# Kernel optimization log

Measured on AMD Instinct MI355X. Metric: run time of the kernel, lower is better.

Reference implementation:

```python
import jax, jax.numpy as jnp
import numpy as np

V, E, H, L, P, N = 500000, 128, 128, 10, 10, 50
SCALE = 1e-4


def setup_inputs() -> dict:
    key = jax.random.key(0)
    ks = jax.random.split(key, 10)
    initrange = 0.5 / E
    return {
        "phr_inds": jax.random.randint(ks[0], (L,), 0, V),
        "pos_inds": jax.random.randint(ks[1], (P, L), 0, V),
        "neg_inds": jax.random.randint(ks[2], (N, L), 0, V),
        "u_emb": jax.random.uniform(ks[3], (V, E), minval=-initrange, maxval=initrange, dtype=jnp.float32),
        "v_emb": jax.random.uniform(ks[4], (V, E), minval=-initrange, maxval=initrange, dtype=jnp.float32),
        "w_ih": jax.random.uniform(ks[5], (3 * H, E), minval=-SCALE, maxval=SCALE, dtype=jnp.float32),
        "w_hh": jax.random.uniform(ks[6], (3 * H, H), minval=-SCALE, maxval=SCALE, dtype=jnp.float32),
        "b_ih": jax.random.uniform(ks[7], (3 * H,), minval=-SCALE, maxval=SCALE, dtype=jnp.float32),
        "b_hh": jax.random.uniform(ks[8], (3 * H,), minval=-SCALE, maxval=SCALE, dtype=jnp.float32),
        "h0": jax.random.uniform(ks[9], (H,), minval=-SCALE, maxval=SCALE, dtype=jnp.float32),
    }


def _gru_last_hidden(x, h0, w_ih, w_hh, b_ih, b_hh):
    # x: [B, L, E] -> last hidden state [B, H]; torch GRU gate order (r, z, n)
    B = x.shape[0]
    gi = jnp.einsum('ble,ge->blg', x, w_ih) + b_ih  # input projections precomputed [B, L, 3H]
    h = jnp.broadcast_to(h0, (B, h0.shape[-1]))

    def step(h, gi_t):
        gh = h @ w_hh.T + b_hh
        ir, iz, in_ = jnp.split(gi_t, 3, axis=-1)
        hr, hz, hn = jnp.split(gh, 3, axis=-1)
        r = jax.nn.sigmoid(ir + hr)
        z = jax.nn.sigmoid(iz + hz)
        n = jnp.tanh(in_ + r * hn)
        return (1.0 - z) * n + z * h, None

    h, _ = jax.lax.scan(step, h, jnp.swapaxes(gi, 0, 1))  # scan over time
    return h


def reference(phr_inds, pos_inds, neg_inds, u_emb, v_emb, w_ih, w_hh, b_ih, b_hh, h0):
    rnn_size = h0.shape[-1]
    phr_x = u_emb[phr_inds][None]   # [1, L, E] (center phrase uses u table)
    pos_x = v_emb[pos_inds]         # [P, L, E]
    neg_x = v_emb[neg_inds]         # [N, L, E]
    x = jnp.concatenate([phr_x, pos_x, neg_x], axis=0)  # batch all GRU calls together
    enc = _gru_last_hidden(x, h0, w_ih, w_hh, b_ih, b_hh)
    node = enc[0]
    n_pos = pos_inds.shape[0]
    pos_e, neg_e = enc[1:1 + n_pos], enc[1 + n_pos:]
    # dot_product_sum(exp=False): sum_i <node, pos_i> / rnn_size
    pos_loss = ((node * pos_e).sum(-1) / rnn_size).sum()
    # dot_product_sum(exp=True): exp(s) masked to s>0, then summed
    s = (node * neg_e).sum(-1) / rnn_size
    neg_sum = (jnp.exp(s) * (s > 0.0).astype(s.dtype)).sum()
    neg_loss = -jnp.log(1.0 + neg_sum)
    return -(neg_loss + pos_loss)
```

## Files before the change

### kernel.cpp

```cpp
#include <hip/hip_runtime.h>
#include <hip/hip_bf16.h>
#include <math.h>

#define V_SZ 500000
#define E_SZ 128
#define H_SZ 128
#define L_SZ 10
#define P_SZ 10
#define N_SZ 50
#define NSEQ (P_SZ + N_SZ)
#define NBLK 60
#define TPB  384

#define FLAG_STRIDE 16
#define SLOT_STRIDE 16
#define FLAG_MAGIC  0x9E370000u

#define GI_STR 388
#define XS_STR 136
#define SLAB_ROWS 192

typedef __attribute__((ext_vector_type(8))) short bf16x8;
typedef __attribute__((ext_vector_type(4))) float f32x4;

#define MFMA(a, b, c) __builtin_amdgcn_mfma_f32_16x16x32_bf16((a), (b), (c), 0, 0, 0)

__device__ __forceinline__ float sigmoidf(float x) {
    return 1.0f / (1.0f + expf(-x));
}

__device__ __forceinline__ unsigned short f2bf(float f) {
    unsigned u = __float_as_uint(f);
    u += 0x7FFFu + ((u >> 16) & 1u);
    return (unsigned short)(u >> 16);
}

__global__ __launch_bounds__(TPB) void gru_fused(
    const int*   __restrict__ phr_inds,
    const int*   __restrict__ pos_inds,
    const int*   __restrict__ neg_inds,
    const float* __restrict__ u_emb,
    const float* __restrict__ v_emb,
    const float* __restrict__ w_ih,
    const float* __restrict__ w_hh,
    const float* __restrict__ b_ih,
    const float* __restrict__ b_hh,
    const float* __restrict__ h0,
    float*       __restrict__ slots,
    unsigned*    __restrict__ flags,
    float*       __restrict__ out)
{
    __shared__ __align__(16) unsigned short stage[SLAB_ROWS * E_SZ];
    __shared__ __align__(16) unsigned short xs_bf16[2][16 * XS_STR];
    __shared__ __align__(16) float          gi_all[2][16 * GI_STR];
    __shared__ __align__(16) float          gh_s[2][3 * H_SZ];
    __shared__ __align__(16) unsigned short hs_bf16[2][H_SZ];
    __shared__ __align__(16) float          node[2][H_SZ];

    const int bj   = blockIdx.x;
    const int seqB = bj + 1;
    const int t    = threadIdx.x;
    const int lane = t & 63;
    const int wv   = t >> 6;
    const int kg   = lane >> 4;
    const int col  = lane & 15;
    const int arow = wv * 64 + col;

    for (int i = t; i < 2 * L_SZ * 32; i += TPB) {
        const int r  = i >> 5;
        const int e4 = i & 31;
        const int g  = (r < L_SZ) ? 0 : 1;
        const int l  = (r < L_SZ) ? r : r - L_SZ;
        int idx; const float* emb;
        if (g == 0)             { idx = phr_inds[l];                       emb = u_emb; }
        else if (seqB <= P_SZ)  { idx = pos_inds[(seqB - 1) * L_SZ + l];   emb = v_emb; }
        else                    { idx = neg_inds[(seqB - 1 - P_SZ) * L_SZ + l]; emb = v_emb; }
        const float4 v = *reinterpret_cast<const float4*>(emb + (size_t)idx * E_SZ + e4 * 4);
        short4 s4;
        s4.x = (short)f2bf(v.x); s4.y = (short)f2bf(v.y);
        s4.z = (short)f2bf(v.z); s4.w = (short)f2bf(v.w);
        *reinterpret_cast<short4*>((char*)&xs_bf16[g][0] + l * (XS_STR * 2) + e4 * 8) = s4;
    }

    const int gseq = t >> 7;
    const int gu   = t & 127;
    float bih_r = 0.f, bih_z = 0.f, bih_n = 0.f;
    float bhh_r = 0.f, bhh_z = 0.f, bhh_n = 0.f;
    float h_reg = 0.f;
    if (t < 2 * H_SZ) {
        bih_r = b_ih[gu]; bih_z = b_ih[gu + 128]; bih_n = b_ih[gu + 256];
        bhh_r = b_hh[gu]; bhh_z = b_hh[gu + 128]; bhh_n = b_hh[gu + 256];
        h_reg = h0[gu];
        hs_bf16[gseq][gu] = f2bf(h_reg);
    }

    bf16x8 aih[4][4], ahh[4][4];
    #pragma unroll
    for (int m = 0; m < 2; ++m) {
        const float* W = (m == 0) ? w_ih : w_hh;
        #pragma unroll
        for (int s = 0; s < 2; ++s) {
            #pragma unroll 8
            for (int q = 0; q < (SLAB_ROWS * E_SZ / 4) / TPB; ++q) {
                const int fi = q * TPB + t;
                const int lr = fi >> 5;
                const int e4 = fi & 31;
                const float4 v = *reinterpret_cast<const float4*>(
                    W + (size_t)(s * SLAB_ROWS + lr) * E_SZ + e4 * 4);
                short4 s4;
                s4.x = (short)f2bf(v.x); s4.y = (short)f2bf(v.y);
                s4.z = (short)f2bf(v.z); s4.w = (short)f2bf(v.w);
                const int byte = (lr * 256 + e4 * 8) ^ ((lr & 7) << 4);
                *reinterpret_cast<short4*>((char*)stage + byte) = s4;
            }
            __syncthreads();

            if (wv >= s * 3 && wv < (s + 1) * 3) {
                const int lr0 = arow - s * SLAB_ROWS;
                #pragma unroll
                for (int mb = 0; mb < 4; ++mb) {
                    #pragma unroll
                    for (int kb = 0; kb < 4; ++kb) {
                        const int lr   = lr0 + mb * 16;
                        const int byte = (lr * 256 + kb * 64 + kg * 16) ^ ((lr & 7) << 4);
                        const bf16x8 f = *reinterpret_cast<const bf16x8*>((const char*)stage + byte);
                        if (m == 0) aih[mb][kb] = f;
                        else        ahh[mb][kb] = f;
                    }
                }
            }
            __syncthreads();
        }
    }

    #pragma unroll
    for (int g = 0; g < 2; ++g) {
        f32x4 g0 = {0.f,0.f,0.f,0.f}, g1 = {0.f,0.f,0.f,0.f};
        f32x4 g2 = {0.f,0.f,0.f,0.f}, g3 = {0.f,0.f,0.f,0.f};
        #pragma unroll
        for (int kb = 0; kb < 4; ++kb) {
            const bf16x8 xb = *reinterpret_cast<const bf16x8*>(
                (const char*)&xs_bf16[g][0] + col * (XS_STR * 2) + kb * 64 + kg * 16);
            g0 = MFMA(aih[0][kb], xb, g0);
            g1 = MFMA(aih[1][kb], xb, g1);
            g2 = MFMA(aih[2][kb], xb, g2);
            g3 = MFMA(aih[3][kb], xb, g3);
        }
        const int rb = wv * 64 + kg * 4;
        *reinterpret_cast<f32x4*>(&gi_all[g][col * GI_STR + rb     ]) = g0;
        *reinterpret_cast<f32x4*>(&gi_all[g][col * GI_STR + rb + 16]) = g1;
        *reinterpret_cast<f32x4*>(&gi_all[g][col * GI_STR + rb + 32]) = g2;
        *reinterpret_cast<f32x4*>(&gi_all[g][col * GI_STR + rb + 48]) = g3;
    }

    for (int l = 0; l < L_SZ; ++l) {
        f32x4 a0 = {0.f,0.f,0.f,0.f}, a1 = {0.f,0.f,0.f,0.f};
        f32x4 a2 = {0.f,0.f,0.f,0.f}, a3 = {0.f,0.f,0.f,0.f};
        #pragma unroll
        for (int kb = 0; kb < 4; ++kb) {
            const bf16x8 bh = *reinterpret_cast<const bf16x8*>(
                (const char*)&hs_bf16[col & 1][0] + kb * 64 + kg * 16);
            a0 = MFMA(ahh[0][kb], bh, a0);
            a1 = MFMA(ahh[1][kb], bh, a1);
            a2 = MFMA(ahh[2][kb], bh, a2);
            a3 = MFMA(ahh[3][kb], bh, a3);
        }
        if (col < 2) {
            const int rb = wv * 64 + kg * 4;
            *reinterpret_cast<f32x4*>(&gh_s[col][rb     ]) = a0;
            *reinterpret_cast<f32x4*>(&gh_s[col][rb + 16]) = a1;
            *reinterpret_cast<f32x4*>(&gh_s[col][rb + 32]) = a2;
            *reinterpret_cast<f32x4*>(&gh_s[col][rb + 48]) = a3;
        }
        __syncthreads();

        if (t < 2 * H_SZ) {
            const float* gi = &gi_all[gseq][l * GI_STR];
            const float* gh = &gh_s[gseq][0];
            const float r = sigmoidf(gi[gu      ] + bih_r + (gh[gu      ] + bhh_r));
            const float z = sigmoidf(gi[gu + 128] + bih_z + (gh[gu + 128] + bhh_z));
            const float n = tanhf  (gi[gu + 256] + bih_n + r * (gh[gu + 256] + bhh_n));
            h_reg = (1.0f - z) * n + z * h_reg;
            if (l < L_SZ - 1) hs_bf16[gseq][gu] = f2bf(h_reg);
            else              node[gseq][gu]   = h_reg;
        }
        __syncthreads();
    }

    if (t >= 64) return;

    float d = node[0][t] * node[1][t] + node[0][t + 64] * node[1][t + 64];
    #pragma unroll
    for (int off = 32; off > 0; off >>= 1) d += __shfl_down(d, off);
    const float s_own = d * (1.0f / (float)H_SZ);

    if (bj != 0) {
        if (t == 0) {
            slots[bj * SLOT_STRIDE] = s_own;
            __threadfence();
            atomicExch(&flags[bj * FLAG_STRIDE], FLAG_MAGIC + (unsigned)bj);
        }
        return;
    }

    float sv = 0.0f;
    if (t == 0) sv = s_own;
    else if (t < NSEQ) {
        const unsigned want = FLAG_MAGIC + (unsigned)t;
        while (atomicAdd(&flags[t * FLAG_STRIDE], 0u) != want) {
            __builtin_amdgcn_s_sleep(2);
        }
        __threadfence();
        sv = slots[t * SLOT_STRIDE];
    }

    float vp = 0.0f, vn = 0.0f;
    if (t < P_SZ)      vp = sv;
    else if (t < NSEQ) vn = (sv > 0.0f) ? expf(sv) : 0.0f;

    #pragma unroll
    for (int off = 32; off > 0; off >>= 1) {
        vp += __shfl_down(vp, off);
        vn += __shfl_down(vn, off);
    }
    if (t == 0) {
        out[0] = logf(1.0f + vn) - vp;
    }
}

extern "C" void kernel_launch(void* const* d_in, const int* in_sizes, int n_in,
                              void* d_out, int out_size, void* d_ws, size_t ws_size,
                              hipStream_t stream) {
    const int*   phr_inds = (const int*)  d_in[0];
    const int*   pos_inds = (const int*)  d_in[1];
    const int*   neg_inds = (const int*)  d_in[2];
    const float* u_emb    = (const float*)d_in[3];
    const float* v_emb    = (const float*)d_in[4];
    const float* w_ih     = (const float*)d_in[5];
    const float* w_hh     = (const float*)d_in[6];
    const float* b_ih     = (const float*)d_in[7];
    const float* b_hh     = (const float*)d_in[8];
    const float* h0       = (const float*)d_in[9];

    float*    slots = (float*)d_ws;
    unsigned* flags = (unsigned*)((char*)d_ws + 16384);

    gru_fused<<<NBLK, TPB, 0, stream>>>(phr_inds, pos_inds, neg_inds,
                                        u_emb, v_emb, w_ih, w_hh, b_ih, b_hh, h0,
                                        slots, flags, (float*)d_out);
}
```

Measured before the change: 23.02 us.

## Repartition GRU gates per wave so gate math stays in registers, one barrier per step

Switches to 8 waves, each owning 16 hidden units across all three gates (r,z,n). The gate nonlinearities are then computed directly from MFMA accumulators in the lanes that hold them, instead of round-tripping gh through shared memory with a second barrier. The hidden state is double-buffered so each timestep needs a single __syncthreads. Weight staging is done in one full 384-row pass per matrix, gi is stored with biases folded in, and the gi buffer reuses the staging LDS. This risks more threads per block and heavier per-lane elementwise work, since only 2 of 16 columns do the gate math.

After: 32.53 us. 41.3% more time.

```diff
diff --git a/kernel.cpp b/kernel.cpp
--- a/kernel.cpp
+++ b/kernel.cpp
@@ -10,15 +10,14 @@
 #define N_SZ 50
 #define NSEQ (P_SZ + N_SZ)
 #define NBLK 60
-#define TPB  384
+#define TPB  512
 
 #define FLAG_STRIDE 16
 #define SLOT_STRIDE 16
 #define FLAG_MAGIC  0x9E370000u
 
-#define GI_STR 388
-#define XS_STR 136
-#define SLAB_ROWS 192
+#define XS_STR  136
+#define GI_USTR 132
 
 typedef __attribute__((ext_vector_type(8))) short bf16x8;
 typedef __attribute__((ext_vector_type(4))) float f32x4;
@@ -50,12 +49,12 @@
     unsigned*    __restrict__ flags,
     float*       __restrict__ out)
 {
-    __shared__ __align__(16) unsigned short stage[SLAB_ROWS * E_SZ];
+    __shared__ __align__(16) unsigned short stage_u[384 * E_SZ];
     __shared__ __align__(16) unsigned short xs_bf16[2][16 * XS_STR];
-    __shared__ __align__(16) float          gi_all[2][16 * GI_STR];
-    __shared__ __align__(16) float          gh_s[2][3 * H_SZ];
-    __shared__ __align__(16) unsigned short hs_bf16[2][H_SZ];
+    __shared__ __align__(16) unsigned short hs_bf16[2][2][H_SZ];
     __shared__ __align__(16) float          node[2][H_SZ];
+
+    float* gi_all = (float*)stage_u;
 
     const int bj   = blockIdx.x;
     const int seqB = bj + 1;
@@ -64,7 +63,8 @@
     const int wv   = t >> 6;
     const int kg   = lane >> 4;
     const int col  = lane & 15;
-    const int arow = wv * 64 + col;
+    const int ur   = wv * 16;
+    const int ub   = ur + kg * 4;
 
     for (int i = t; i < 2 * L_SZ * 32; i += TPB) {
         const int r  = i >> 5;
@@ -82,109 +82,107 @@
         *reinterpret_cast<short4*>((char*)&xs_bf16[g][0] + l * (XS_STR * 2) + e4 * 8) = s4;
     }
 
-    const int gseq = t >> 7;
-    const int gu   = t & 127;
-    float bih_r = 0.f, bih_z = 0.f, bih_n = 0.f;
-    float bhh_r = 0.f, bhh_z = 0.f, bhh_n = 0.f;
-    float h_reg = 0.f;
-    if (t < 2 * H_SZ) {
-        bih_r = b_ih[gu]; bih_z = b_ih[gu + 128]; bih_n = b_ih[gu + 256];
-        bhh_r = b_hh[gu]; bhh_z = b_hh[gu + 128]; bhh_n = b_hh[gu + 256];
-        h_reg = h0[gu];
-        hs_bf16[gseq][gu] = f2bf(h_reg);
-    }
-
-    bf16x8 aih[4][4], ahh[4][4];
+    const f32x4 bihr = *reinterpret_cast<const f32x4*>(b_ih + ub);
+    const f32x4 bihz = *reinterpret_cast<const f32x4*>(b_ih + 128 + ub);
+    const f32x4 bihn = *reinterpret_cast<const f32x4*>(b_ih + 256 + ub);
+    const f32x4 bhhr = *reinterpret_cast<const f32x4*>(b_hh + ub);
+    const f32x4 bhhz = *reinterpret_cast<const f32x4*>(b_hh + 128 + ub);
+    const f32x4 bhhn = *reinterpret_cast<const f32x4*>(b_hh + 256 + ub);
+    f32x4 hreg = *reinterpret_cast<const f32x4*>(h0 + ub);
+
+    if (col < 2) {
+        short4 s4;
+        s4.x = (short)f2bf(hreg[0]); s4.y = (short)f2bf(hreg[1]);
+        s4.z = (short)f2bf(hreg[2]); s4.w = (short)f2bf(hreg[3]);
+        *reinterpret_cast<short4*>(&hs_bf16[0][col][ub]) = s4;
+    }
+
+    bf16x8 aih[3][4], ahh[3][4];
     #pragma unroll
     for (int m = 0; m < 2; ++m) {
         const float* W = (m == 0) ? w_ih : w_hh;
+        #pragma unroll 8
+        for (int q = 0; q < (384 * E_SZ / 4) / TPB; ++q) {
+            const int fi = q * TPB + t;
+            const int lr = fi >> 5;
+            const int e4 = fi & 31;
+            const float4 v = *reinterpret_cast<const float4*>(W + (size_t)lr * E_SZ + e4 * 4);
+            short4 s4;
+            s4.x = (short)f2bf(v.x); s4.y = (short)f2bf(v.y);
+            s4.z = (short)f2bf(v.z); s4.w = (short)f2bf(v.w);
+            const int byte = (lr * 256 + e4 * 8) ^ ((lr & 7) << 4);
+            *reinterpret_cast<short4*>((char*)stage_u + byte) = s4;
+        }
+        __syncthreads();
+
         #pragma unroll
-        for (int s = 0; s < 2; ++s) {
-            #pragma unroll 8
-            for (int q = 0; q < (SLAB_ROWS * E_SZ / 4) / TPB; ++q) {
-                const int fi = q * TPB + t;
-                const int lr = fi >> 5;
-                const int e4 = fi & 31;
-                const float4 v = *reinterpret_cast<const float4*>(
-                    W + (size_t)(s * SLAB_ROWS + lr) * E_SZ + e4 * 4);
-                short4 s4;
-                s4.x = (short)f2bf(v.x); s4.y = (short)f2bf(v.y);
-                s4.z = (short)f2bf(v.z); s4.w = (short)f2bf(v.w);
-                const int byte = (lr * 256 + e4 * 8) ^ ((lr & 7) << 4);
-                *reinterpret_cast<short4*>((char*)stage + byte) = s4;
+        for (int gate = 0; gate < 3; ++gate) {
+            const int lr = gate * H_SZ + ur + col;
+            #pragma unroll
+            for (int kb = 0; kb < 4; ++kb) {
+                const int byte = (lr * 256 + kb * 64 + kg * 16) ^ ((lr & 7) << 4);
+                const bf16x8 f = *reinterpret_cast<const bf16x8*>((const char*)stage_u + byte);
+                if (m == 0) aih[gate][kb] = f;
+                else        ahh[gate][kb] = f;
             }
-            __syncthreads();
-
-            if (wv >= s * 3 && wv < (s + 1) * 3) {
-                const int lr0 = arow - s * SLAB_ROWS;
-                #pragma unroll
-                for (int mb = 0; mb < 4; ++mb) {
-                    #pragma unroll
-                    for (int kb = 0; kb < 4; ++kb) {
-                        const int lr   = lr0 + mb * 16;
-                        const int byte = (lr * 256 + kb * 64 + kg * 16) ^ ((lr & 7) << 4);
-                        const bf16x8 f = *reinterpret_cast<const bf16x8*>((const char*)stage + byte);
-                        if (m == 0) aih[mb][kb] = f;
-                        else        ahh[mb][kb] = f;
-                    }
-                }
-            }
-            __syncthreads();
-        }
+        }
+        __syncthreads();
     }
 
     #pragma unroll
     for (int g = 0; g < 2; ++g) {
-        f32x4 g0 = {0.f,0.f,0.f,0.f}, g1 = {0.f,0.f,0.f,0.f};
-        f32x4 g2 = {0.f,0.f,0.f,0.f}, g3 = {0.f,0.f,0.f,0.f};
+        f32x4 ar = {0.f,0.f,0.f,0.f}, az = {0.f,0.f,0.f,0.f}, an = {0.f,0.f,0.f,0.f};
         #pragma unroll
         for (int kb = 0; kb < 4; ++kb) {
             const bf16x8 xb = *reinterpret_cast<const bf16x8*>(
                 (const char*)&xs_bf16[g][0] + col * (XS_STR * 2) + kb * 64 + kg * 16);
-            g0 = MFMA(aih[0][kb], xb, g0);
-            g1 = MFMA(aih[1][kb], xb, g1);
-            g2 = MFMA(aih[2][kb], xb, g2);
-            g3 = MFMA(aih[3][kb], xb, g3);
-        }
-        const int rb = wv * 64 + kg * 4;
-        *reinterpret_cast<f32x4*>(&gi_all[g][col * GI_STR + rb     ]) = g0;
-        *reinterpret_cast<f32x4*>(&gi_all[g][col * GI_STR + rb + 16]) = g1;
-        *reinterpret_cast<f32x4*>(&gi_all[g][col * GI_STR + rb + 32]) = g2;
-        *reinterpret_cast<f32x4*>(&gi_all[g][col * GI_STR + rb + 48]) = g3;
-    }
-
+            ar = MFMA(aih[0][kb], xb, ar);
+            az = MFMA(aih[1][kb], xb, az);
+            an = MFMA(aih[2][kb], xb, an);
+        }
+        if (col < L_SZ) {
+            const int base = (g * L_SZ + col) * 3;
+            *reinterpret_cast<f32x4*>(&gi_all[(base + 0) * GI_USTR + ub]) = ar + bihr;
+            *reinterpret_cast<f32x4*>(&gi_all[(base + 1) * GI_USTR + ub]) = az + bihz;
+            *reinterpret_cast<f32x4*>(&gi_all[(base + 2) * GI_USTR + ub]) = an + bihn;
+        }
+    }
+    __syncthreads();
+
+    int p = 0;
     for (int l = 0; l < L_SZ; ++l) {
-        f32x4 a0 = {0.f,0.f,0.f,0.f}, a1 = {0.f,0.f,0.f,0.f};
-        f32x4 a2 = {0.f,0.f,0.f,0.f}, a3 = {0.f,0.f,0.f,0.f};
+        f32x4 ar = {0.f,0.f,0.f,0.f}, az = {0.f,0.f,0.f,0.f}, an = {0.f,0.f,0.f,0.f};
         #pragma unroll
         for (int kb = 0; kb < 4; ++kb) {
             const bf16x8 bh = *reinterpret_cast<const bf16x8*>(
-                (const char*)&hs_bf16[col & 1][0] + kb * 64 + kg * 16);
-            a0 = MFMA(ahh[0][kb], bh, a0);
-            a1 = MFMA(ahh[1][kb], bh, a1);
-            a2 = MFMA(ahh[2][kb], bh, a2);
-            a3 = MFMA(ahh[3][kb], bh, a3);
+                (const char*)&hs_bf16[p][col & 1][0] + kb * 64 + kg * 16);
+            ar = MFMA(ahh[0][kb], bh, ar);
+            az = MFMA(ahh[1][kb], bh, az);
+            an = MFMA(ahh[2][kb], bh, an);
         }
         if (col < 2) {
-            const int rb = wv * 64 + kg * 4;
-            *reinterpret_cast<f32x4*>(&gh_s[col][rb     ]) = a0;
-            *reinterpret_cast<f32x4*>(&gh_s[col][rb + 16]) = a1;
-            *reinterpret_cast<f32x4*>(&gh_s[col][rb + 32]) = a2;
-            *reinterpret_cast<f32x4*>(&gh_s[col][rb + 48]) = a3;
+            const int base = (col * L_SZ + l) * 3;
+            const f32x4 gr = *reinterpret_cast<const f32x4*>(&gi_all[(base + 0) * GI_USTR + ub]);
+            const f32x4 gz = *reinterpret_cast<const f32x4*>(&gi_all[(base + 1) * GI_USTR + ub]);
+            const f32x4 gn = *reinterpret_cast<const f32x4*>(&gi_all[(base + 2) * GI_USTR + ub]);
+            #pragma unroll
+            for (int j = 0; j < 4; ++j) {
+                const float r = sigmoidf(gr[j] + (ar[j] + bhhr[j]));
+                const float z = sigmoidf(gz[j] + (az[j] + bhhz[j]));
+                const float n = tanhf  (gn[j] + r * (an[j] + bhhn[j]));
+                hreg[j] = (1.0f - z) * n + z * hreg[j];
+            }
+            if (l < L_SZ - 1) {
+                short4 s4;
+                s4.x = (short)f2bf(hreg[0]); s4.y = (short)f2bf(hreg[1]);
+                s4.z = (short)f2bf(hreg[2]); s4.w = (short)f2bf(hreg[3]);
+                *reinterpret_cast<short4*>(&hs_bf16[p ^ 1][col][ub]) = s4;
+            } else {
+                *reinterpret_cast<f32x4*>(&node[col][ub]) = hreg;
+            }
         }
         __syncthreads();
-
-        if (t < 2 * H_SZ) {
-            const float* gi = &gi_all[gseq][l * GI_STR];
-            const float* gh = &gh_s[gseq][0];
-            const float r = sigmoidf(gi[gu      ] + bih_r + (gh[gu      ] + bhh_r));
-            const float z = sigmoidf(gi[gu + 128] + bih_z + (gh[gu + 128] + bhh_z));
-            const float n = tanhf  (gi[gu + 256] + bih_n + r * (gh[gu + 256] + bhh_n));
-            h_reg = (1.0f - z) * n + z * h_reg;
-            if (l < L_SZ - 1) hs_bf16[gseq][gu] = f2bf(h_reg);
-            else              node[gseq][gu]   = h_reg;
-        }
-        __syncthreads();
+        p ^= 1;
     }
 
     if (t >= 64) return;
```
